# Kernel tuning notes

Measured on AMD Instinct MI355X. Metric: run time of the kernel, lower is better.

Reference implementation:

```python
import jax, jax.numpy as jnp
from jax import lax
import numpy as np

NB_CODE = 16384
DIM = 128
SCALES = [(1, 1), (2, 2), (4, 4), (8, 8), (16, 16)]
PHI_IDX = [0, 1, 1, 2, 3]  # PhiPartiallyShared: argmin(|ticks - si/(SN-1)|), K=4, SN=5
RESI = 0.5  # abs(quant_resi)
BETA = 0.25


def _cubic(x, a=-0.75):
    # PyTorch bicubic kernel (cubic convolution, a=-0.75)
    ax = np.abs(x)
    return np.where(ax <= 1.0, (a + 2.0) * ax ** 3 - (a + 3.0) * ax ** 2 + 1.0,
                    np.where(ax < 2.0, a * ax ** 3 - 5.0 * a * ax ** 2 + 8.0 * a * ax - 4.0 * a, 0.0))


def bicubic_mat(n_in, n_out):
    # 1D interpolation matrix matching torch F.interpolate(mode='bicubic', align_corners=False)
    W = np.zeros((n_out, n_in), dtype=np.float32)
    scale = n_in / n_out
    for i in range(n_out):
        x = (i + 0.5) * scale - 0.5
        x0 = int(np.floor(x))
        t = x - x0
        for k in range(4):
            idx = min(max(x0 - 1 + k, 0), n_in - 1)  # border clamp
            W[i, idx] += _cubic(t + 1.0 - k)
    return jnp.asarray(W)


def phi_apply(h, w, b):
    y = lax.conv_general_dilated(h, w, (1, 1), 'SAME',
                                 dimension_numbers=('NCHW', 'OIHW', 'NCHW'))
    y = y + b[None, :, None, None]
    return h * (1.0 - RESI) + y * RESI


def setup_inputs() -> dict:
    key = jax.random.key(0)
    k1, k2, k3, k4 = jax.random.split(key, 4)
    B, C, J, L = 16, DIM, 16, 16
    f_bcjl = jax.random.normal(k1, (B, C, J, L), dtype=jnp.float32)
    emb = jax.random.normal(k2, (NB_CODE, C), dtype=jnp.float32) * 0.02
    # 4 partially-shared Phi convs (3x3, C->C)
    phi_w = jax.random.normal(k3, (4, C, C, 3, 3), dtype=jnp.float32) * (1.0 / np.sqrt(C * 9))
    phi_b = jax.random.normal(k4, (4, C), dtype=jnp.float32) * 0.01
    return {'f_bcjl': f_bcjl, 'emb': emb, 'phi_w': phi_w, 'phi_b': phi_b}


def reference(f_bcjl, emb, phi_w, phi_b):
    B, C, J, L = f_bcjl.shape
    SN = len(SCALES)
    f_ng = lax.stop_gradient(f_bcjl)
    f_rest = f_ng
    f_hat = jnp.zeros_like(f_ng)
    loss = jnp.float32(0.0)
    e_sq = jnp.sum(emb * emb, axis=1)  # [K]
    idx_all = []
    for si, (sn, tn) in enumerate(SCALES):
        if si != SN - 1:
            # 'area' downsample == integer-factor average pooling here
            r = f_rest.reshape(B, C, sn, J // sn, tn, L // tn).mean(axis=(3, 5))
        else:
            r = f_rest
        rNC = r.transpose(0, 2, 3, 1).reshape(-1, C)  # [N, C]
        d = jnp.sum(rNC * rNC, axis=1, keepdims=True) + e_sq - 2.0 * (rNC @ emb.T)
        idx = jnp.argmin(d, axis=1)  # [N]
        idx_all.append(idx)
        h = emb[idx].reshape(B, sn, tn, C).transpose(0, 3, 1, 2)  # [B,C,sn,tn]
        if si != SN - 1:
            Wj = bicubic_mat(sn, J)
            Wl = bicubic_mat(tn, L)
            h = jnp.einsum('js,bcst,lt->bcjl', Wj, h, Wl)
        k = PHI_IDX[si]
        h = phi_apply(h, phi_w[k], phi_b[k])
        f_hat = f_hat + h
        f_rest = f_rest - h
        loss = loss + BETA * jnp.mean((lax.stop_gradient(f_hat) - f_bcjl) ** 2) \
                    + jnp.mean((f_hat - f_ng) ** 2)
    loss = loss / SN
    idx_cat = jnp.concatenate(idx_all)
    counts = jnp.zeros((NB_CODE,), jnp.float32).at[idx_cat].add(1.0)
    p = counts / idx_cat.shape[0]
    perplexity = jnp.exp(-jnp.sum(p * jnp.log(p + 1e-10)))
    # straight-through estimator
    f_hat_out = lax.stop_gradient(f_hat) - f_ng + f_bcjl
    return (f_hat_out, loss, perplexity)
```

## Files before the change

kernel.cpp:

```cpp
#include <hip/hip_runtime.h>
#include <hip/hip_bf16.h>
#include <math.h>

#define BATCH 16
#define CDIM  128
#define NCODE 16384
#define ELEMS 524288
#define NTOT  5456
#define WEXT_TOT 589824
#define LOSS_COEF 4.76837158203125e-7f

typedef __attribute__((ext_vector_type(8))) short short8;
typedef __attribute__((ext_vector_type(4))) float float4v;
typedef unsigned short ushortT;
typedef unsigned long long u64;
typedef unsigned int u32;

__device__ __forceinline__ ushortT f2bf(float x) {
    __hip_bfloat16 h = __float2bfloat16(x);
    return *reinterpret_cast<ushortT*>(&h);
}
__device__ __forceinline__ float bf2f(ushortT b) {
    __hip_bfloat16 h = *reinterpret_cast<__hip_bfloat16*>(&b);
    return __bfloat162float(h);
}
__device__ __forceinline__ u32 ford(float v) {
    u32 b = __float_as_uint(v);
    return b ^ ((u32)((int)b >> 31) | 0x80000000u);
}

__device__ double cubic_d(double x) {
    const double a = -0.75;
    double ax = fabs(x);
    if (ax <= 1.0) return (a + 2.0) * ax * ax * ax - (a + 3.0) * ax * ax + 1.0;
    if (ax < 2.0)  return a * ax * ax * ax - 5.0 * a * ax * ax + 8.0 * a * ax - 4.0 * a;
    return 0.0;
}

__global__ __launch_bounds__(256)
void k_prologue(const float* __restrict__ f, const float* __restrict__ emb,
                const float* __restrict__ phi_w,
                float* __restrict__ f_rest, float* __restrict__ f_hat,
                float* __restrict__ esq, ushortT* __restrict__ embext,
                ushortT* __restrict__ wext, float* __restrict__ wmat,
                float* __restrict__ lossA, ushortT* __restrict__ rext,
                u64* __restrict__ packed) {
    __shared__ float red[4];
    const int t = threadIdx.x;
    const int bid = blockIdx.x;
    const int id = bid * 256 + t;

    if (bid < 2048) {
        float fv = f[id];
        f_rest[id] = fv;
        f_hat[id] = 0.f;
        int row = id >> 5, c4 = id & 31;
        float4 v = reinterpret_cast<const float4*>(emb + (size_t)row * CDIM)[c4];
        float xs[4] = {v.x, v.y, v.z, v.w};
        ushortT hi[4], lo[4];
        float ss = 0.f;
        #pragma unroll
        for (int i = 0; i < 4; ++i) {
            hi[i] = f2bf(xs[i]);
            lo[i] = f2bf(xs[i] - bf2f(hi[i]));
            ss += xs[i] * xs[i];
        }
        ushortT* base = embext + (size_t)row * 256;
        *reinterpret_cast<ushort4*>(base + c4 * 4)       = make_ushort4(hi[0], hi[1], hi[2], hi[3]);
        *reinterpret_cast<ushort4*>(base + 128 + c4 * 4) = make_ushort4(lo[0], lo[1], lo[2], lo[3]);
        #pragma unroll
        for (int off = 16; off; off >>= 1) ss += __shfl_down(ss, off);
        if ((t & 31) == 0) esq[row] = ss;

        float s = fv;
        #pragma unroll
        for (int off = 32; off; off >>= 1) s += __shfl_down(s, off);
        if ((t & 63) == 0) red[t >> 6] = s;
        __syncthreads();
        if (t == 0) {
            float m = (red[0] + red[1] + red[2] + red[3]) * (1.f / 256.f);
            int b = bid >> 7, c = bid & 127;
            ushortT h = f2bf(m);
            rext[b * 256 + c] = h;
            rext[b * 256 + 128 + c] = f2bf(m - bf2f(h));
        }
    } else {
        int idz = (bid - 2048) * 256 + t;
        if (idz < 30720)
            reinterpret_cast<u32*>(rext + 16 * 256)[idz] = 0;
    }
    if (id < WEXT_TOT) {
        int k4 = id / 147456, rem = id % 147456;
        int co = rem / 1152, kk = rem % 1152;
        int off = kk >> 7, ci = kk & 127;
        float v = 0.5f * phi_w[(((size_t)(k4 * 128 + co)) * 128 + ci) * 9 + off];
        if (ci == co && off == 4) v += 0.5f;
        wext[id] = f2bf(v);
    }
    if (bid == 0 && t < 64) {
        int sIdx = t >> 4;
        int S = 1 << sIdx;
        int j = t & 15;
        const int offs[4] = {0, 16, 48, 112};
        double row[8];
        for (int s = 0; s < 8; ++s) row[s] = 0.0;
        double scale = (double)S / 16.0;
        double x = (j + 0.5) * scale - 0.5;
        double x0 = floor(x);
        double tt = x - x0;
        for (int k = 0; k < 4; ++k) {
            int idx = (int)x0 - 1 + k;
            idx = idx < 0 ? 0 : (idx > S - 1 ? S - 1 : idx);
            row[idx] += cubic_d(tt + 1.0 - k);
        }
        for (int s = 0; s < S; ++s) wmat[offs[sIdx] + j * S + s] = (float)row[s];
    }
    if (id == 0) lossA[0] = 0.f;
    if (id < 8192) packed[id] = ~0ull;
}

__global__ __launch_bounds__(256)
void k_packext(const float* __restrict__ fr, ushortT* __restrict__ re,
               int N, int padN, int S, int lgS) {
    int id = blockIdx.x * 256 + threadIdx.x;
    if (id >= padN * 32) return;
    int row = id >> 5, c4 = id & 31;
    ushortT hi[4], lo[4];
    if (row < N) {
        int mask = S - 1;
        int tt = row & mask, ssi = (row >> lgS) & mask, b = row >> (2 * lgS);
        int bs = 16 >> lgS;
        float inv = 1.f / (float)(bs * bs);
        #pragma unroll
        for (int u = 0; u < 4; ++u) {
            int c = c4 * 4 + u;
            const float* base = fr + (size_t)(b * 128 + c) * 256 + (ssi * bs) * 16 + tt * bs;
            float acc = 0.f;
            for (int jj = 0; jj < bs; ++jj)
                for (int ll = 0; ll < bs; ++ll)
                    acc += base[jj * 16 + ll];
            float x = acc * inv;
            hi[u] = f2bf(x);
            lo[u] = f2bf(x - bf2f(hi[u]));
        }
    } else {
        #pragma unroll
        for (int u = 0; u < 4; ++u) { hi[u] = 0; lo[u] = 0; }
    }
    ushortT* base = re + (size_t)row * 256;
    *reinterpret_cast<ushort4*>(base + c4 * 4)       = make_ushort4(hi[0], hi[1], hi[2], hi[3]);
    *reinterpret_cast<ushort4*>(base + 128 + c4 * 4) = make_ushort4(lo[0], lo[1], lo[2], lo[3]);
}

__global__ __launch_bounds__(256)
void k_packext_wave(const float* __restrict__ fr, ushortT* __restrict__ re,
                    int N, int padN, int S, int lgS) {
    int gid = blockIdx.x * 256 + threadIdx.x;
    int wid = gid >> 6, lane = threadIdx.x & 63;
    if (wid >= padN * 128) return;
    int row = wid >> 7, c = wid & 127;
    float x = 0.f;
    if (row < N) {
        int mask = S - 1;
        int tt = row & mask, ssi = (row >> lgS) & mask, b = row >> (2 * lgS);
        int lgbs = 4 - lgS, bs = 1 << lgbs, cnt = bs * bs;
        const float* base = fr + (size_t)(b * 128 + c) * 256 + (ssi * bs) * 16 + tt * bs;
        float acc = 0.f;
        for (int e = lane; e < cnt; e += 64)
            acc += base[(e >> lgbs) * 16 + (e & (bs - 1))];
        #pragma unroll
        for (int off = 32; off; off >>= 1) acc += __shfl_down(acc, off);
        x = acc / (float)cnt;
    }
    if (lane == 0) {
        ushortT h = f2bf(x);
        re[(size_t)row * 256 + c] = h;
        re[(size_t)row * 256 + 128 + c] = f2bf(x - bf2f(h));
    }
}

__global__ __launch_bounds__(256)
void k_argmin_mfma(const ushortT* __restrict__ rext, const ushortT* __restrict__ embext,
                   const float* __restrict__ esq, int N, int kPerSplit, int KS,
                   u64* __restrict__ packed) {
    __shared__ ushortT Btile[2][64 * 32 * 8];
    const int t = threadIdx.x;
    const int w = t >> 6;
    const int lane = t & 63;
    const int ln = lane & 15;
    const int q  = lane >> 4;
    const int bid = blockIdx.x;
    const int ky = bid % KS;
    const int rb = bid / KS;
    const int k0beg = ky * kPerSplit;
    const int rowW = rb * 128 + w * 32;

    short8 a[2][8];
    #pragma unroll
    for (int ti = 0; ti < 2; ++ti) {
        const ushortT* r0 = rext + (size_t)(rowW + ti * 16 + ln) * 256 + q * 8;
        #pragma unroll
        for (int sb = 0; sb < 8; ++sb)
            a[ti][sb] = *reinterpret_cast<const short8*>(r0 + sb * 32);
    }

    float minv[2][4];
    int   mini[2][4];
    #pragma unroll
    for (int ti = 0; ti < 2; ++ti)
        #pragma unroll
        for (int rg = 0; rg < 4; ++rg) { minv[ti][rg] = 3.4e38f; mini[ti][rg] = 0; }

    const int tiles = kPerSplit >> 6;

    #pragma unroll
    for (int i = 0; i < 8; ++i) {
        int F = (i * 4 + w) * 64 + lane;
        int n = F >> 5, cs = F & 31;
        int cp = (cs & ~7) | ((cs & 7) ^ (n & 7));
        const ushortT* src = embext + (size_t)(k0beg + n) * 256 + cp * 8;
        __builtin_amdgcn_global_load_lds(
            (const __attribute__((address_space(1))) unsigned int*)src,
            (__attribute__((address_space(3))) unsigned int*)&Btile[0][(size_t)((i * 4 + w) * 64) * 8],
            16, 0, 0);
    }

    for (int it = 0; it < tiles; ++it) {
        __syncthreads();
        if (it + 1 < tiles) {
            int k1 = k0beg + (it + 1) * 64;
            int bu = (it + 1) & 1;
            #pragma unroll
            for (int i = 0; i < 8; ++i) {
                int F = (i * 4 + w) * 64 + lane;
                int n = F >> 5, cs = F & 31;
                int cp = (cs & ~7) | ((cs & 7) ^ (n & 7));
                const ushortT* src = embext + (size_t)(k1 + n) * 256 + cp * 8;
                __builtin_amdgcn_global_load_lds(
                    (const __attribute__((address_space(1))) unsigned int*)src,
                    (__attribute__((address_space(3))) unsigned int*)&Btile[bu][(size_t)((i * 4 + w) * 64) * 8],
                    16, 0, 0);
            }
        }
        const ushortT* Bt = Btile[it & 1];
        const int k0 = k0beg + it * 64;

        #pragma unroll
        for (int sub = 0; sub < 4; ++sub) {
            int n = sub * 16 + ln;
            short8 bfr[8];
            #pragma unroll
            for (int sb = 0; sb < 8; ++sb) {
                int cp = q + 4 * sb;
                int cs = (cp & ~7) | ((cp & 7) ^ (n & 7));
                bfr[sb] = *reinterpret_cast<const short8*>(&Bt[(size_t)(n * 32 + cs) * 8]);
            }
            float4v acc[2];
            #pragma unroll
            for (int ti = 0; ti < 2; ++ti) acc[ti] = (float4v){0.f, 0.f, 0.f, 0.f};
            #pragma unroll
            for (int s = 0; s < 12; ++s) {
                int as = s < 8 ? s : s - 8;
                int bs = s < 4 ? s : s - 4;
                #pragma unroll
                for (int ti = 0; ti < 2; ++ti)
                    acc[ti] = __builtin_amdgcn_mfma_f32_16x16x32_bf16(a[ti][as], bfr[bs], acc[ti], 0, 0, 0);
            }
            int kc = k0 + sub * 16 + ln;
            float es = esq[kc];
            #pragma unroll
            for (int ti = 0; ti < 2; ++ti)
                #pragma unroll
                for (int rg = 0; rg < 4; ++rg) {
                    float sc = fmaf(-2.f, acc[ti][rg], es);
                    if (sc < minv[ti][rg]) { minv[ti][rg] = sc; mini[ti][rg] = kc; }
                }
        }
    }

    #pragma unroll
    for (int ti = 0; ti < 2; ++ti)
        #pragma unroll
        for (int rg = 0; rg < 4; ++rg) {
            float v = minv[ti][rg]; int ix = mini[ti][rg];
            #pragma unroll
            for (int off = 1; off < 16; off <<= 1) {
                float ov = __shfl_xor(v, off);
                int   oi = __shfl_xor(ix, off);
                if (ov < v || (ov == v && oi < ix)) { v = ov; ix = oi; }
            }
            if (ln == 0) {
                int row = rowW + ti * 16 + q * 4 + rg;
                if (row < N) {
                    u64 p = ((u64)ford(v) << 32) | (u32)ix;
                    atomicMin(&packed[row], p);
                }
            }
        }
}

__global__ __launch_bounds__(256)
void k_upconv(const float* __restrict__ emb, const u64* __restrict__ packed,
              const float* __restrict__ wm, int S, int lastScale,
              const ushortT* __restrict__ wext, const float* __restrict__ bias,
              const float* __restrict__ f_in, float* __restrict__ f_hat,
              float* __restrict__ f_rest, float* __restrict__ loss_acc,
              int storeRest, int packNext, ushortT* __restrict__ rext_out) {
    __shared__ __align__(16) ushortT Htile[3 * 16 * 128];
    __shared__ __align__(16) float tmpS[3 * 8 * 128];
    __shared__ float wsum[4];
    const int t = threadIdx.x;
    const int b = blockIdx.x >> 4;
    const int j = blockIdx.x & 15;
    const int l = t >> 4, c8 = t & 15;
    const int phys = (c8 & 8) | ((c8 & 7) ^ (l & 7));

    if (lastScale) {
        #pragma unroll
        for (int r = 0; r < 3; ++r) {
            int jin = j - 1 + r;
            float acc[8] = {0.f, 0.f, 0.f, 0.f, 0.f, 0.f, 0.f, 0.f};
            if (jin >= 0 && jin < 16) {
                int idx = (int)(u32)(packed[(b * 16 + jin) * 16 + l] & 0xFFFFFFFFull);
                const float* er = emb + (size_t)idx * CDIM + c8 * 8;
                float4 e0 = *reinterpret_cast<const float4*>(er);
                float4 e1 = *reinterpret_cast<const float4*>(er + 4);
                acc[0] = e0.x; acc[1] = e0.y; acc[2] = e0.z; acc[3] = e0.w;
                acc[4] = e1.x; acc[5] = e1.y; acc[6] = e1.z; acc[7] = e1.w;
            }
            short8 o;
            #pragma unroll
            for (int i = 0; i < 8; ++i) o[i] = (short)f2bf(acc[i]);
            *reinterpret_cast<short8*>(&Htile[((size_t)(r * 16 + l) * 16 + phys) * 8]) = o;
        }
    } else {
        int items = 3 * S * 16;
        for (int i = t; i < items; i += 256) {
            int r = i / (S * 16);
            int rem = i - r * (S * 16);
            int t2 = rem >> 4, cc8 = rem & 15;
            int jin = j - 1 + r;
            float a0[8] = {0.f, 0.f, 0.f, 0.f, 0.f, 0.f, 0.f, 0.f};
            if (jin >= 0 && jin < 16) {
                for (int s = 0; s < S; ++s) {
                    float wjv = wm[jin * S + s];
                    int idx = (int)(u32)(packed[b * S * S + s * S + t2] & 0xFFFFFFFFull);
                    const float* er = emb + (size_t)idx * CDIM + cc8 * 8;
                    float4 e0 = *reinterpret_cast<const float4*>(er);
                    float4 e1 = *reinterpret_cast<const float4*>(er + 4);
                    a0[0] += wjv * e0.x; a0[1] += wjv * e0.y;
                    a0[2] += wjv * e0.z; a0[3] += wjv * e0.w;
                    a0[4] += wjv * e1.x; a0[5] += wjv * e1.y;
                    a0[6] += wjv * e1.z; a0[7] += wjv * e1.w;
                }
            }
            float* tp = &tmpS[((size_t)(r * 8 + t2)) * 128 + cc8 * 8];
            *reinterpret_cast<float4*>(tp)     = make_float4(a0[0], a0[1], a0[2], a0[3]);
            *reinterpret_cast<float4*>(tp + 4) = make_float4(a0[4], a0[5], a0[6], a0[7]);
        }
        __syncthreads();
        #pragma unroll
        for (int r = 0; r < 3; ++r) {
            float acc[8] = {0.f, 0.f, 0.f, 0.f, 0.f, 0.f, 0.f, 0.f};
            for (int t2 = 0; t2 < S; ++t2) {
                float wlv = wm[l * S + t2];
                const float* tp = &tmpS[((size_t)(r * 8 + t2)) * 128 + c8 * 8];
                float4 v0 = *reinterpret_cast<const float4*>(tp);
                float4 v1 = *reinterpret_cast<const float4*>(tp + 4);
                acc[0] += wlv * v0.x; acc[1] += wlv * v0.y;
                acc[2] += wlv * v0.z; acc[3] += wlv * v0.w;
                acc[4] += wlv * v1.x; acc[5] += wlv * v1.y;
                acc[6] += wlv * v1.z; acc[7] += wlv * v1.w;
            }
            short8 o;
            #pragma unroll
            for (int i = 0; i < 8; ++i) o[i] = (short)f2bf(acc[i]);
            *reinterpret_cast<short8*>(&Htile[((size_t)(r * 16 + l) * 16 + phys) * 8]) = o;
        }
    }
    __syncthreads();

    const int w = t >> 6, lane = t & 63;
    const int ln = lane & 15, q = lane >> 4;
    const int co0 = w * 32;
    const ushortT* wA = wext + (size_t)(co0 + ln) * 1152;
    float4v acc2[2] = {{0.f, 0.f, 0.f, 0.f}, {0.f, 0.f, 0.f, 0.f}};
    const short8 zz = {0, 0, 0, 0, 0, 0, 0, 0};

    #pragma unroll 3
    for (int off = 0; off < 9; ++off) {
        const int dj = off / 3, dl = off % 3;
        int cIn = ln + dl - 1;
        int cCl = cIn < 0 ? 0 : (cIn > 15 ? 15 : cIn);
        bool oob = (cIn != cCl);
        int rb = (dj * 16 + cCl) * 128;
        #pragma unroll
        for (int g = 0; g < 4; ++g) {
            int csl = g * 4 + q;
            int ph2 = (csl & 8) | ((csl & 7) ^ (cCl & 7));
            short8 av = *reinterpret_cast<const short8*>(&Htile[rb + ph2 * 8]);
            if (oob) av = zz;
            const ushortT* wr = wA + (off * 4 + g) * 32 + q * 8;
            short8 b0 = *reinterpret_cast<const short8*>(wr);
            short8 b1 = *reinterpret_cast<const short8*>(wr + 16 * 1152);
            acc2[0] = __builtin_amdgcn_mfma_f32_16x16x32_bf16(av, b0, acc2[0], 0, 0, 0);
            acc2[1] = __builtin_amdgcn_mfma_f32_16x16x32_bf16(av, b1, acc2[1], 0, 0, 0);
        }
    }

    float s = 0.f;
    #pragma unroll
    for (int sn = 0; sn < 2; ++sn) {
        int co = co0 + sn * 16 + ln;
        float bsv = 0.5f * bias[co];
        size_t gi = ((size_t)(b * 128 + co) * 16 + j) * 16 + q * 4;
        float4 fh = *reinterpret_cast<const float4*>(&f_hat[gi]);
        float4 fv = *reinterpret_cast<const float4*>(&f_in[gi]);
        float oo[4] = {acc2[sn][0] + bsv, acc2[sn][1] + bsv,
                       acc2[sn][2] + bsv, acc2[sn][3] + bsv};
        float fhv[4] = {fh.x + oo[0], fh.y + oo[1], fh.z + oo[2], fh.w + oo[3]};
        *reinterpret_cast<float4*>(&f_hat[gi]) =
            make_float4(fhv[0], fhv[1], fhv[2], fhv[3]);
        float fvv[4] = {fv.x, fv.y, fv.z, fv.w};
        #pragma unroll
        for (int i = 0; i < 4; ++i) {
            float d = fhv[i] - fvv[i];
            s += d * d;
        }
        if (storeRest || packNext) {
            float4 fr = *reinterpret_cast<const float4*>(&f_rest[gi]);
            float frn[4] = {fr.x - oo[0], fr.y - oo[1], fr.z - oo[2], fr.w - oo[3]};
            if (storeRest)
                *reinterpret_cast<float4*>(&f_rest[gi]) =
                    make_float4(frn[0], frn[1], frn[2], frn[3]);
            if (packNext) {
                #pragma unroll
                for (int i = 0; i < 4; ++i) {
                    int row = b * 256 + j * 16 + q * 4 + i;
                    ushortT hv = f2bf(frn[i]);
                    rext_out[(size_t)row * 256 + co] = hv;
                    rext_out[(size_t)row * 256 + 128 + co] = f2bf(frn[i] - bf2f(hv));
                }
            }
        }
    }
    #pragma unroll
    for (int off = 32; off; off >>= 1) s += __shfl_down(s, off);
    if (lane == 0) wsum[w] = s;
    __syncthreads();
    if (t == 0)
        atomicAdd(loss_acc, (wsum[0] + wsum[1] + wsum[2] + wsum[3]) * LOSS_COEF);
}

__global__ __launch_bounds__(256)
void k_final(const u64* __restrict__ packed, const float* __restrict__ loss_acc,
             float* __restrict__ out) {
    __shared__ u32 cnt2[NCODE / 2];
    __shared__ float ws4[4];
    int t = threadIdx.x;
    for (int i = t; i < NCODE / 2; i += 256) cnt2[i] = 0;
    __syncthreads();
    for (int i = t; i < NTOT; i += 256) {
        int idx = (int)(u32)(packed[i] & 0xFFFFFFFFull);
        atomicAdd(&cnt2[idx >> 1], (idx & 1) ? 65536u : 1u);
    }
    __syncthreads();
    float s = 0.f;
    for (int k = t; k < NCODE; k += 256) {
        u32 c = cnt2[k >> 1];
        c = (k & 1) ? (c >> 16) : (c & 0xFFFFu);
        float p = (float)c * (1.0f / (float)NTOT);
        s += p * logf(p + 1e-10f);
    }
    #pragma unroll
    for (int off = 32; off; off >>= 1) s += __shfl_down(s, off);
    if ((t & 63) == 0) ws4[t >> 6] = s;
    __syncthreads();
    if (t == 0) {
        out[ELEMS]     = loss_acc[0];
        out[ELEMS + 1] = expf(-(ws4[0] + ws4[1] + ws4[2] + ws4[3]));
    }
}

extern "C" void kernel_launch(void* const* d_in, const int* in_sizes, int n_in,
                              void* d_out, int out_size, void* d_ws, size_t ws_size,
                              hipStream_t stream) {
    const float* f     = (const float*)d_in[0];
    const float* emb   = (const float*)d_in[1];
    const float* phi_w = (const float*)d_in[2];
    const float* phi_b = (const float*)d_in[3];
    float* out = (float*)d_out;

    float* wsf = (float*)d_ws;
    float*   f_rest = wsf;
    float*   esq    = wsf + 524288;
    float*   wmat   = wsf + 540672;
    float*   lossA  = wsf + 540928;
    u64*     packed = (u64*)(wsf + 540992);
    ushortT* embext = (ushortT*)(wsf + 557376);
    ushortT* rext   = (ushortT*)(wsf + 2654528);
    ushortT* wext   = (ushortT*)(wsf + 3178816);

    k_prologue<<<2304, 256, 0, stream>>>(f, emb, phi_w, f_rest, out, esq,
                                         embext, wext, wmat, lossA, rext, packed);

    const int Ss[5]     = {1, 2, 4, 8, 16};
    const int lgSs[5]   = {0, 1, 2, 3, 4};
    const int phiIdx[5] = {0, 1, 1, 2, 3};
    const int ksplit[5] = {256, 256, 128, 64, 16};
    const int wmOff[5]  = {0, 16, 48, 112, 0};
    const int pOff[5]   = {0, 16, 80, 336, 1360};

    for (int si = 0; si < 5; ++si) {
        int S = Ss[si], lgS = lgSs[si];
        int N = 16 * S * S;
        int padN = (N + 127) & ~127;
        u64* pk = packed + pOff[si];

        if (si == 1)
            k_packext_wave<<<padN * 128 / 4, 256, 0, stream>>>(f_rest, rext, N, padN, S, lgS);
        else if (si == 2 || si == 3)
            k_packext<<<padN * 32 / 256, 256, 0, stream>>>(f_rest, rext, N, padN, S, lgS);

        int KS = ksplit[si];
        k_argmin_mfma<<<(padN / 128) * KS, 256, 0, stream>>>(rext, embext, esq,
                                                             N, NCODE / KS, KS, pk);

        int k = phiIdx[si];
        k_upconv<<<256, 256, 0, stream>>>(emb, pk, wmat + wmOff[si], S, si == 4 ? 1 : 0,
                                          wext + (size_t)k * 147456,
                                          phi_b + (size_t)k * 128, f, out, f_rest, lossA,
                                          si <= 2 ? 1 : 0, si == 3 ? 1 : 0, rext);
    }

    k_final<<<1, 256, 0, stream>>>(packed, lossA, out);
}
```

Measured before the change: 320.2 us.

## Fuse all stages into one persistent cooperative kernel with grid syncs

Replaces the chain of roughly fifteen kernel launches (prologue, pack, argmin, upconv per scale, final) with a single cooperative persistent kernel that loops over jobs and uses grid.sync between stages. The goal is to remove launch overhead and inter-kernel gaps, which are large relative to the small per-scale work. The argmin's double-buffered LDS prefetch is dropped for a single buffer so the shared memory fits two blocks per CU, which gives up overlap between loads and MFMA work. The old multi-kernel path stays as a fallback if the cooperative launch is unavailable or fails.

```diff
diff --git a/kernel.cpp b/kernel.cpp
--- a/kernel.cpp
+++ b/kernel.cpp
@@ -1,8 +1,10 @@
 #include <hip/hip_runtime.h>
+#include <hip/hip_cooperative_groups.h>
 #include <hip/hip_bf16.h>
 #include <math.h>
 
-#define BATCH 16
+namespace cg = cooperative_groups;
+
 #define CDIM  128
 #define NCODE 16384
 #define ELEMS 524288
@@ -28,7 +30,6 @@
     u32 b = __float_as_uint(v);
     return b ^ ((u32)((int)b >> 31) | 0x80000000u);
 }
-
 __device__ double cubic_d(double x) {
     const double a = -0.75;
     double ax = fabs(x);
@@ -37,161 +38,18 @@
     return 0.0;
 }
 
-__global__ __launch_bounds__(256)
-void k_prologue(const float* __restrict__ f, const float* __restrict__ emb,
-                const float* __restrict__ phi_w,
-                float* __restrict__ f_rest, float* __restrict__ f_hat,
-                float* __restrict__ esq, ushortT* __restrict__ embext,
-                ushortT* __restrict__ wext, float* __restrict__ wmat,
-                float* __restrict__ lossA, ushortT* __restrict__ rext,
-                u64* __restrict__ packed) {
-    __shared__ float red[4];
-    const int t = threadIdx.x;
-    const int bid = blockIdx.x;
-    const int id = bid * 256 + t;
-
-    if (bid < 2048) {
-        float fv = f[id];
-        f_rest[id] = fv;
-        f_hat[id] = 0.f;
-        int row = id >> 5, c4 = id & 31;
-        float4 v = reinterpret_cast<const float4*>(emb + (size_t)row * CDIM)[c4];
-        float xs[4] = {v.x, v.y, v.z, v.w};
-        ushortT hi[4], lo[4];
-        float ss = 0.f;
-        #pragma unroll
-        for (int i = 0; i < 4; ++i) {
-            hi[i] = f2bf(xs[i]);
-            lo[i] = f2bf(xs[i] - bf2f(hi[i]));
-            ss += xs[i] * xs[i];
-        }
-        ushortT* base = embext + (size_t)row * 256;
-        *reinterpret_cast<ushort4*>(base + c4 * 4)       = make_ushort4(hi[0], hi[1], hi[2], hi[3]);
-        *reinterpret_cast<ushort4*>(base + 128 + c4 * 4) = make_ushort4(lo[0], lo[1], lo[2], lo[3]);
-        #pragma unroll
-        for (int off = 16; off; off >>= 1) ss += __shfl_down(ss, off);
-        if ((t & 31) == 0) esq[row] = ss;
-
-        float s = fv;
-        #pragma unroll
-        for (int off = 32; off; off >>= 1) s += __shfl_down(s, off);
-        if ((t & 63) == 0) red[t >> 6] = s;
-        __syncthreads();
-        if (t == 0) {
-            float m = (red[0] + red[1] + red[2] + red[3]) * (1.f / 256.f);
-            int b = bid >> 7, c = bid & 127;
-            ushortT h = f2bf(m);
-            rext[b * 256 + c] = h;
-            rext[b * 256 + 128 + c] = f2bf(m - bf2f(h));
-        }
-    } else {
-        int idz = (bid - 2048) * 256 + t;
-        if (idz < 30720)
-            reinterpret_cast<u32*>(rext + 16 * 256)[idz] = 0;
-    }
-    if (id < WEXT_TOT) {
-        int k4 = id / 147456, rem = id % 147456;
-        int co = rem / 1152, kk = rem % 1152;
-        int off = kk >> 7, ci = kk & 127;
-        float v = 0.5f * phi_w[(((size_t)(k4 * 128 + co)) * 128 + ci) * 9 + off];
-        if (ci == co && off == 4) v += 0.5f;
-        wext[id] = f2bf(v);
-    }
-    if (bid == 0 && t < 64) {
-        int sIdx = t >> 4;
-        int S = 1 << sIdx;
-        int j = t & 15;
-        const int offs[4] = {0, 16, 48, 112};
-        double row[8];
-        for (int s = 0; s < 8; ++s) row[s] = 0.0;
-        double scale = (double)S / 16.0;
-        double x = (j + 0.5) * scale - 0.5;
-        double x0 = floor(x);
-        double tt = x - x0;
-        for (int k = 0; k < 4; ++k) {
-            int idx = (int)x0 - 1 + k;
-            idx = idx < 0 ? 0 : (idx > S - 1 ? S - 1 : idx);
-            row[idx] += cubic_d(tt + 1.0 - k);
-        }
-        for (int s = 0; s < S; ++s) wmat[offs[sIdx] + j * S + s] = (float)row[s];
-    }
-    if (id == 0) lossA[0] = 0.f;
-    if (id < 8192) packed[id] = ~0ull;
-}
-
-__global__ __launch_bounds__(256)
-void k_packext(const float* __restrict__ fr, ushortT* __restrict__ re,
-               int N, int padN, int S, int lgS) {
-    int id = blockIdx.x * 256 + threadIdx.x;
-    if (id >= padN * 32) return;
-    int row = id >> 5, c4 = id & 31;
-    ushortT hi[4], lo[4];
-    if (row < N) {
-        int mask = S - 1;
-        int tt = row & mask, ssi = (row >> lgS) & mask, b = row >> (2 * lgS);
-        int bs = 16 >> lgS;
-        float inv = 1.f / (float)(bs * bs);
-        #pragma unroll
-        for (int u = 0; u < 4; ++u) {
-            int c = c4 * 4 + u;
-            const float* base = fr + (size_t)(b * 128 + c) * 256 + (ssi * bs) * 16 + tt * bs;
-            float acc = 0.f;
-            for (int jj = 0; jj < bs; ++jj)
-                for (int ll = 0; ll < bs; ++ll)
-                    acc += base[jj * 16 + ll];
-            float x = acc * inv;
-            hi[u] = f2bf(x);
-            lo[u] = f2bf(x - bf2f(hi[u]));
-        }
-    } else {
-        #pragma unroll
-        for (int u = 0; u < 4; ++u) { hi[u] = 0; lo[u] = 0; }
-    }
-    ushortT* base = re + (size_t)row * 256;
-    *reinterpret_cast<ushort4*>(base + c4 * 4)       = make_ushort4(hi[0], hi[1], hi[2], hi[3]);
-    *reinterpret_cast<ushort4*>(base + 128 + c4 * 4) = make_ushort4(lo[0], lo[1], lo[2], lo[3]);
-}
-
-__global__ __launch_bounds__(256)
-void k_packext_wave(const float* __restrict__ fr, ushortT* __restrict__ re,
-                    int N, int padN, int S, int lgS) {
-    int gid = blockIdx.x * 256 + threadIdx.x;
-    int wid = gid >> 6, lane = threadIdx.x & 63;
-    if (wid >= padN * 128) return;
-    int row = wid >> 7, c = wid & 127;
-    float x = 0.f;
-    if (row < N) {
-        int mask = S - 1;
-        int tt = row & mask, ssi = (row >> lgS) & mask, b = row >> (2 * lgS);
-        int lgbs = 4 - lgS, bs = 1 << lgbs, cnt = bs * bs;
-        const float* base = fr + (size_t)(b * 128 + c) * 256 + (ssi * bs) * 16 + tt * bs;
-        float acc = 0.f;
-        for (int e = lane; e < cnt; e += 64)
-            acc += base[(e >> lgbs) * 16 + (e & (bs - 1))];
-        #pragma unroll
-        for (int off = 32; off; off >>= 1) acc += __shfl_down(acc, off);
-        x = acc / (float)cnt;
-    }
-    if (lane == 0) {
-        ushortT h = f2bf(x);
-        re[(size_t)row * 256 + c] = h;
-        re[(size_t)row * 256 + 128 + c] = f2bf(x - bf2f(h));
-    }
-}
-
-__global__ __launch_bounds__(256)
-void k_argmin_mfma(const ushortT* __restrict__ rext, const ushortT* __restrict__ embext,
-                   const float* __restrict__ esq, int N, int kPerSplit, int KS,
-                   u64* __restrict__ packed) {
-    __shared__ ushortT Btile[2][64 * 32 * 8];
-    const int t = threadIdx.x;
+
+__device__ __forceinline__
+void dev_argmin_sb(char* smem, int jid, const ushortT* __restrict__ rext,
+                   const ushortT* __restrict__ embext, const float* __restrict__ esq,
+                   int N, int kPerSplit, int KS, u64* __restrict__ packed, int t) {
+    ushortT* B0 = reinterpret_cast<ushortT*>(smem);
     const int w = t >> 6;
     const int lane = t & 63;
     const int ln = lane & 15;
     const int q  = lane >> 4;
-    const int bid = blockIdx.x;
-    const int ky = bid % KS;
-    const int rb = bid / KS;
+    const int ky = jid % KS;
+    const int rb = jid / KS;
     const int k0beg = ky * kPerSplit;
     const int rowW = rb * 128 + w * 32;
 
@@ -212,38 +70,21 @@
         for (int rg = 0; rg < 4; ++rg) { minv[ti][rg] = 3.4e38f; mini[ti][rg] = 0; }
 
     const int tiles = kPerSplit >> 6;
-
-    #pragma unroll
-    for (int i = 0; i < 8; ++i) {
-        int F = (i * 4 + w) * 64 + lane;
-        int n = F >> 5, cs = F & 31;
-        int cp = (cs & ~7) | ((cs & 7) ^ (n & 7));
-        const ushortT* src = embext + (size_t)(k0beg + n) * 256 + cp * 8;
-        __builtin_amdgcn_global_load_lds(
-            (const __attribute__((address_space(1))) unsigned int*)src,
-            (__attribute__((address_space(3))) unsigned int*)&Btile[0][(size_t)((i * 4 + w) * 64) * 8],
-            16, 0, 0);
-    }
-
     for (int it = 0; it < tiles; ++it) {
         __syncthreads();
-        if (it + 1 < tiles) {
-            int k1 = k0beg + (it + 1) * 64;
-            int bu = (it + 1) & 1;
-            #pragma unroll
-            for (int i = 0; i < 8; ++i) {
-                int F = (i * 4 + w) * 64 + lane;
-                int n = F >> 5, cs = F & 31;
-                int cp = (cs & ~7) | ((cs & 7) ^ (n & 7));
-                const ushortT* src = embext + (size_t)(k1 + n) * 256 + cp * 8;
-                __builtin_amdgcn_global_load_lds(
-                    (const __attribute__((address_space(1))) unsigned int*)src,
-                    (__attribute__((address_space(3))) unsigned int*)&Btile[bu][(size_t)((i * 4 + w) * 64) * 8],
-                    16, 0, 0);
-            }
-        }
-        const ushortT* Bt = Btile[it & 1];
-        const int k0 = k0beg + it * 64;
+        int k0 = k0beg + it * 64;
+        #pragma unroll
+        for (int i = 0; i < 8; ++i) {
+            int F = (i * 4 + w) * 64 + lane;
+            int n = F >> 5, cs = F & 31;
+            int cp = (cs & ~7) | ((cs & 7) ^ (n & 7));
+            const ushortT* src = embext + (size_t)(k0 + n) * 256 + cp * 8;
+            __builtin_amdgcn_global_load_lds(
+                (const __attribute__((address_space(1))) unsigned int*)src,
+                (__attribute__((address_space(3))) unsigned int*)&B0[(size_t)((i * 4 + w) * 64) * 8],
+                16, 0, 0);
+        }
+        __syncthreads();
 
         #pragma unroll
         for (int sub = 0; sub < 4; ++sub) {
@@ -253,7 +94,7 @@
             for (int sb = 0; sb < 8; ++sb) {
                 int cp = q + 4 * sb;
                 int cs = (cp & ~7) | ((cp & 7) ^ (n & 7));
-                bfr[sb] = *reinterpret_cast<const short8*>(&Bt[(size_t)(n * 32 + cs) * 8]);
+                bfr[sb] = *reinterpret_cast<const short8*>(&B0[(size_t)(n * 32 + cs) * 8]);
             }
             float4v acc[2];
             #pragma unroll
@@ -299,19 +140,19 @@
         }
 }
 
-__global__ __launch_bounds__(256)
-void k_upconv(const float* __restrict__ emb, const u64* __restrict__ packed,
-              const float* __restrict__ wm, int S, int lastScale,
-              const ushortT* __restrict__ wext, const float* __restrict__ bias,
-              const float* __restrict__ f_in, float* __restrict__ f_hat,
-              float* __restrict__ f_rest, float* __restrict__ loss_acc,
-              int storeRest, int packNext, ushortT* __restrict__ rext_out) {
-    __shared__ __align__(16) ushortT Htile[3 * 16 * 128];
-    __shared__ __align__(16) float tmpS[3 * 8 * 128];
-    __shared__ float wsum[4];
-    const int t = threadIdx.x;
-    const int b = blockIdx.x >> 4;
-    const int j = blockIdx.x & 15;
+__device__ __forceinline__
+void dev_upconv(char* smem, int job, const float* __restrict__ emb,
+                const u64* __restrict__ packed, const float* __restrict__ wm,
+                int S, int lastScale, const ushortT* __restrict__ wext,
+                const float* __restrict__ bias, const float* __restrict__ f_in,
+                float* __restrict__ f_hat, float* __restrict__ f_rest,
+                float* __restrict__ loss_acc, int storeRest, int packNext,
+                ushortT* __restrict__ rext_out, int t) {
+    ushortT* Htile = reinterpret_cast<ushortT*>(smem);
+    float*   tmpS  = reinterpret_cast<float*>(smem + 12288);
+    float*   wsum  = reinterpret_cast<float*>(smem + 24576);
+    const int b = job >> 4;
+    const int j = job & 15;
     const int l = t >> 4, c8 = t & 15;
     const int phys = (c8 & 8) | ((c8 & 7) ^ (l & 7));
 
@@ -452,6 +293,375 @@
         atomicAdd(loss_acc, (wsum[0] + wsum[1] + wsum[2] + wsum[3]) * LOSS_COEF);
 }
 
+__global__ __launch_bounds__(256, 2)
+void k_mega(const float* __restrict__ f, const float* __restrict__ emb,
+            const float* __restrict__ phi_w, const float* __restrict__ phi_b,
+            float* __restrict__ out, float* __restrict__ f_rest,
+            float* __restrict__ esq, float* __restrict__ wmat,
+            float* __restrict__ lossA, u64* __restrict__ packed,
+            ushortT* __restrict__ embext, ushortT* __restrict__ rext,
+            ushortT* __restrict__ wext) {
+    cg::grid_group grid = cg::this_grid();
+    __shared__ __align__(16) char smem[32768];
+    const int t = threadIdx.x;
+    const int bid = blockIdx.x;
+    const int NB = gridDim.x;
+
+    {
+        float* red = reinterpret_cast<float*>(smem);
+        for (int base = bid * 256; base < WEXT_TOT; base += NB * 256) {
+            int id = base + t;
+            if (base < ELEMS) {
+                float fv = f[id];
+                f_rest[id] = fv;
+                out[id] = 0.f;
+                int row = id >> 5, c4 = id & 31;
+                float4 v = reinterpret_cast<const float4*>(emb + (size_t)row * CDIM)[c4];
+                float xs[4] = {v.x, v.y, v.z, v.w};
+                ushortT hi[4], lo[4];
+                float ss = 0.f;
+                #pragma unroll
+                for (int i = 0; i < 4; ++i) {
+                    hi[i] = f2bf(xs[i]);
+                    lo[i] = f2bf(xs[i] - bf2f(hi[i]));
+                    ss += xs[i] * xs[i];
+                }
+                ushortT* basep = embext + (size_t)row * 256;
+                *reinterpret_cast<ushort4*>(basep + c4 * 4)       = make_ushort4(hi[0], hi[1], hi[2], hi[3]);
+                *reinterpret_cast<ushort4*>(basep + 128 + c4 * 4) = make_ushort4(lo[0], lo[1], lo[2], lo[3]);
+                #pragma unroll
+                for (int off = 16; off; off >>= 1) ss += __shfl_down(ss, off);
+                if ((t & 31) == 0) esq[row] = ss;
+
+                float s = fv;
+                #pragma unroll
+                for (int off = 32; off; off >>= 1) s += __shfl_down(s, off);
+                if ((t & 63) == 0) red[t >> 6] = s;
+                __syncthreads();
+                if (t == 0) {
+                    float m = (red[0] + red[1] + red[2] + red[3]) * (1.f / 256.f);
+                    int plane = base >> 8;
+                    int b = plane >> 7, c = plane & 127;
+                    ushortT h = f2bf(m);
+                    rext[b * 256 + c] = h;
+                    rext[b * 256 + 128 + c] = f2bf(m - bf2f(h));
+                }
+                __syncthreads();
+            }
+            if (id < WEXT_TOT) {
+                int k4 = id / 147456, rem = id % 147456;
+                int co = rem / 1152, kk = rem % 1152;
+                int off = kk >> 7, ci = kk & 127;
+                float v = 0.5f * phi_w[(((size_t)(k4 * 128 + co)) * 128 + ci) * 9 + off];
+                if (ci == co && off == 4) v += 0.5f;
+                wext[id] = f2bf(v);
+            }
+        }
+        for (int idz = bid * 256 + t; idz < 30720; idz += NB * 256)
+            reinterpret_cast<u32*>(rext + 16 * 256)[idz] = 0;
+        if (bid == 0 && t < 64) {
+            int sIdx = t >> 4;
+            int S = 1 << sIdx;
+            int j = t & 15;
+            const int offs[4] = {0, 16, 48, 112};
+            double row[8];
+            for (int s = 0; s < 8; ++s) row[s] = 0.0;
+            double scale = (double)S / 16.0;
+            double x = (j + 0.5) * scale - 0.5;
+            double x0 = floor(x);
+            double tt = x - x0;
+            for (int k = 0; k < 4; ++k) {
+                int idx = (int)x0 - 1 + k;
+                idx = idx < 0 ? 0 : (idx > S - 1 ? S - 1 : idx);
+                row[idx] += cubic_d(tt + 1.0 - k);
+            }
+            for (int s = 0; s < S; ++s) wmat[offs[sIdx] + j * S + s] = (float)row[s];
+        }
+        if (bid == 0 && t == 0) lossA[0] = 0.f;
+        for (int i = bid * 256 + t; i < 8192; i += NB * 256) packed[i] = ~0ull;
+    }
+    grid.sync();
+
+    const int Ss[5]     = {1, 2, 4, 8, 16};
+    const int phiIdx[5] = {0, 1, 1, 2, 3};
+    const int ksplit[5] = {256, 256, 128, 64, 16};
+    const int wmOff[5]  = {0, 16, 48, 112, 0};
+    const int pOff[5]   = {0, 16, 80, 336, 1360};
+    const int padNs[5]  = {128, 128, 256, 1024, 4096};
+
+    for (int si = 0; si < 5; ++si) {
+        const int S = Ss[si];
+        const int N = 16 * S * S;
+        const int padN = padNs[si];
+        const int KS = ksplit[si];
+        u64* pk = packed + pOff[si];
+
+        if (si == 1) {
+            const int w = t >> 6, lane = t & 63;
+            for (int wj = bid * 4 + w; wj < padN * 128; wj += NB * 4) {
+                int row = wj >> 7, c = wj & 127;
+                float x = 0.f;
+                if (row < N) {
+                    int tt = row & 1, ssi = (row >> 1) & 1, b = row >> 2;
+                    const float* basep = f_rest + (size_t)(b * 128 + c) * 256 + (ssi * 8) * 16 + tt * 8;
+                    float acc = 0.f;
+                    for (int e = lane; e < 64; e += 64)
+                        acc += basep[(e >> 3) * 16 + (e & 7)];
+                    #pragma unroll
+                    for (int off = 32; off; off >>= 1) acc += __shfl_down(acc, off);
+                    x = acc * (1.f / 64.f);
+                }
+                if (lane == 0) {
+                    ushortT h = f2bf(x);
+                    rext[(size_t)row * 256 + c] = h;
+                    rext[(size_t)row * 256 + 128 + c] = f2bf(x - bf2f(h));
+                }
+            }
+            grid.sync();
+        } else if (si == 2 || si == 3) {
+            const int lgS = si;
+            for (int id2 = bid * 256 + t; id2 < padN * 32; id2 += NB * 256) {
+                int row = id2 >> 5, c4 = id2 & 31;
+                ushortT hi[4], lo[4];
+                if (row < N) {
+                    int mask = S - 1;
+                    int tt = row & mask, ssi = (row >> lgS) & mask, b = row >> (2 * lgS);
+                    int bs = 16 >> lgS;
+                    float inv = 1.f / (float)(bs * bs);
+                    #pragma unroll
+                    for (int u = 0; u < 4; ++u) {
+                        int c = c4 * 4 + u;
+                        const float* basep = f_rest + (size_t)(b * 128 + c) * 256 + (ssi * bs) * 16 + tt * bs;
+                        float acc = 0.f;
+                        for (int jj = 0; jj < bs; ++jj)
+                            for (int ll = 0; ll < bs; ++ll)
+                                acc += basep[jj * 16 + ll];
+                        float x = acc * inv;
+                        hi[u] = f2bf(x);
+                        lo[u] = f2bf(x - bf2f(hi[u]));
+                    }
+                } else {
+                    #pragma unroll
+                    for (int u = 0; u < 4; ++u) { hi[u] = 0; lo[u] = 0; }
+                }
+                ushortT* basep = rext + (size_t)row * 256;
+                *reinterpret_cast<ushort4*>(basep + c4 * 4)       = make_ushort4(hi[0], hi[1], hi[2], hi[3]);
+                *reinterpret_cast<ushort4*>(basep + 128 + c4 * 4) = make_ushort4(lo[0], lo[1], lo[2], lo[3]);
+            }
+            grid.sync();
+        }
+
+        {
+            int njobs = (padN / 128) * KS;
+            for (int jid = bid; jid < njobs; jid += NB)
+                dev_argmin_sb(smem, jid, rext, embext, esq, N, NCODE / KS, KS, pk, t);
+            grid.sync();
+        }
+
+        {
+            int k = phiIdx[si];
+            for (int job = bid; job < 256; job += NB)
+                dev_upconv(smem, job, emb, pk, wmat + wmOff[si], S, si == 4 ? 1 : 0,
+                           wext + (size_t)k * 147456, phi_b + (size_t)k * 128,
+                           f, out, f_rest, lossA,
+                           si <= 2 ? 1 : 0, si == 3 ? 1 : 0, rext, t);
+            grid.sync();
+        }
+    }
+
+    if (bid == 0) {
+        u32* cnt2 = reinterpret_cast<u32*>(smem);
+        for (int i = t; i < NCODE / 2; i += 256) cnt2[i] = 0;
+        __syncthreads();
+        for (int i = t; i < NTOT; i += 256) {
+            int idx = (int)(u32)(packed[i] & 0xFFFFFFFFull);
+            atomicAdd(&cnt2[idx >> 1], (idx & 1) ? 65536u : 1u);
+        }
+        __syncthreads();
+        float s = 0.f;
+        for (int k = t; k < NCODE; k += 256) {
+            u32 c = cnt2[k >> 1];
+            c = (k & 1) ? (c >> 16) : (c & 0xFFFFu);
+            float p = (float)c * (1.0f / (float)NTOT);
+            s += p * logf(p + 1e-10f);
+        }
+        __syncthreads();
+        float* ws4 = reinterpret_cast<float*>(smem);
+        #pragma unroll
+        for (int off = 32; off; off >>= 1) s += __shfl_down(s, off);
+        if ((t & 63) == 0) ws4[t >> 6] = s;
+        __syncthreads();
+        if (t == 0) {
+            out[ELEMS]     = lossA[0];
+            out[ELEMS + 1] = expf(-(ws4[0] + ws4[1] + ws4[2] + ws4[3]));
+        }
+    }
+}
+
+__global__ __launch_bounds__(256)
+void k_prologue(const float* __restrict__ f, const float* __restrict__ emb,
+                const float* __restrict__ phi_w,
+                float* __restrict__ f_rest, float* __restrict__ f_hat,
+                float* __restrict__ esq, ushortT* __restrict__ embext,
+                ushortT* __restrict__ wext, float* __restrict__ wmat,
+                float* __restrict__ lossA, ushortT* __restrict__ rext,
+                u64* __restrict__ packed) {
+    __shared__ float red[4];
+    const int t = threadIdx.x;
+    const int bid = blockIdx.x;
+    const int id = bid * 256 + t;
+
+    if (bid < 2048) {
+        float fv = f[id];
+        f_rest[id] = fv;
+        f_hat[id] = 0.f;
+        int row = id >> 5, c4 = id & 31;
+        float4 v = reinterpret_cast<const float4*>(emb + (size_t)row * CDIM)[c4];
+        float xs[4] = {v.x, v.y, v.z, v.w};
+        ushortT hi[4], lo[4];
+        float ss = 0.f;
+        #pragma unroll
+        for (int i = 0; i < 4; ++i) {
+            hi[i] = f2bf(xs[i]);
+            lo[i] = f2bf(xs[i] - bf2f(hi[i]));
+            ss += xs[i] * xs[i];
+        }
+        ushortT* base = embext + (size_t)row * 256;
+        *reinterpret_cast<ushort4*>(base + c4 * 4)       = make_ushort4(hi[0], hi[1], hi[2], hi[3]);
+        *reinterpret_cast<ushort4*>(base + 128 + c4 * 4) = make_ushort4(lo[0], lo[1], lo[2], lo[3]);
+        #pragma unroll
+        for (int off = 16; off; off >>= 1) ss += __shfl_down(ss, off);
+        if ((t & 31) == 0) esq[row] = ss;
+
+        float s = fv;
+        #pragma unroll
+        for (int off = 32; off; off >>= 1) s += __shfl_down(s, off);
+        if ((t & 63) == 0) red[t >> 6] = s;
+        __syncthreads();
+        if (t == 0) {
+            float m = (red[0] + red[1] + red[2] + red[3]) * (1.f / 256.f);
+            int b = bid >> 7, c = bid & 127;
+            ushortT h = f2bf(m);
+            rext[b * 256 + c] = h;
+            rext[b * 256 + 128 + c] = f2bf(m - bf2f(h));
+        }
+    } else {
+        int idz = (bid - 2048) * 256 + t;
+        if (idz < 30720)
+            reinterpret_cast<u32*>(rext + 16 * 256)[idz] = 0;
+    }
+    if (id < WEXT_TOT) {
+        int k4 = id / 147456, rem = id % 147456;
+        int co = rem / 1152, kk = rem % 1152;
+        int off = kk >> 7, ci = kk & 127;
+        float v = 0.5f * phi_w[(((size_t)(k4 * 128 + co)) * 128 + ci) * 9 + off];
+        if (ci == co && off == 4) v += 0.5f;
+        wext[id] = f2bf(v);
+    }
+    if (bid == 0 && t < 64) {
+        int sIdx = t >> 4;
+        int S = 1 << sIdx;
+        int j = t & 15;
+        const int offs[4] = {0, 16, 48, 112};
+        double row[8];
+        for (int s = 0; s < 8; ++s) row[s] = 0.0;
+        double scale = (double)S / 16.0;
+        double x = (j + 0.5) * scale - 0.5;
+        double x0 = floor(x);
+        double tt = x - x0;
+        for (int k = 0; k < 4; ++k) {
+            int idx = (int)x0 - 1 + k;
+            idx = idx < 0 ? 0 : (idx > S - 1 ? S - 1 : idx);
+            row[idx] += cubic_d(tt + 1.0 - k);
+        }
+        for (int s = 0; s < S; ++s) wmat[offs[sIdx] + j * S + s] = (float)row[s];
+    }
+    if (id == 0) lossA[0] = 0.f;
+    if (id < 8192) packed[id] = ~0ull;
+}
+
+__global__ __launch_bounds__(256)
+void k_packext(const float* __restrict__ fr, ushortT* __restrict__ re,
+               int N, int padN, int S, int lgS) {
+    int id = blockIdx.x * 256 + threadIdx.x;
+    if (id >= padN * 32) return;
+    int row = id >> 5, c4 = id & 31;
+    ushortT hi[4], lo[4];
+    if (row < N) {
+        int mask = S - 1;
+        int tt = row & mask, ssi = (row >> lgS) & mask, b = row >> (2 * lgS);
+        int bs = 16 >> lgS;
+        float inv = 1.f / (float)(bs * bs);
+        #pragma unroll
+        for (int u = 0; u < 4; ++u) {
+            int c = c4 * 4 + u;
+            const float* base = fr + (size_t)(b * 128 + c) * 256 + (ssi * bs) * 16 + tt * bs;
+            float acc = 0.f;
+            for (int jj = 0; jj < bs; ++jj)
+                for (int ll = 0; ll < bs; ++ll)
+                    acc += base[jj * 16 + ll];
+            float x = acc * inv;
+            hi[u] = f2bf(x);
+            lo[u] = f2bf(x - bf2f(hi[u]));
+        }
+    } else {
+        #pragma unroll
+        for (int u = 0; u < 4; ++u) { hi[u] = 0; lo[u] = 0; }
+    }
+    ushortT* base = re + (size_t)row * 256;
+    *reinterpret_cast<ushort4*>(base + c4 * 4)       = make_ushort4(hi[0], hi[1], hi[2], hi[3]);
+    *reinterpret_cast<ushort4*>(base + 128 + c4 * 4) = make_ushort4(lo[0], lo[1], lo[2], lo[3]);
+}
+
+__global__ __launch_bounds__(256)
+void k_packext_wave(const float* __restrict__ fr, ushortT* __restrict__ re,
+                    int N, int padN, int S, int lgS) {
+    int gid = blockIdx.x * 256 + threadIdx.x;
+    int wid = gid >> 6, lane = threadIdx.x & 63;
+    if (wid >= padN * 128) return;
+    int row = wid >> 7, c = wid & 127;
+    float x = 0.f;
+    if (row < N) {
+        int mask = S - 1;
+        int tt = row & mask, ssi = (row >> lgS) & mask, b = row >> (2 * lgS);
+        int lgbs = 4 - lgS, bs = 1 << lgbs, cnt = bs * bs;
+        const float* base = fr + (size_t)(b * 128 + c) * 256 + (ssi * bs) * 16 + tt * bs;
+        float acc = 0.f;
+        for (int e = lane; e < cnt; e += 64)
+            acc += base[(e >> lgbs) * 16 + (e & (bs - 1))];
+        #pragma unroll
+        for (int off = 32; off; off >>= 1) acc += __shfl_down(acc, off);
+        x = acc / (float)cnt;
+    }
+    if (lane == 0) {
+        ushortT h = f2bf(x);
+        re[(size_t)row * 256 + c] = h;
+        re[(size_t)row * 256 + 128 + c] = f2bf(x - bf2f(h));
+    }
+}
+
+__global__ __launch_bounds__(256)
+void k_argmin_fb(const ushortT* __restrict__ rext, const ushortT* __restrict__ embext,
+                 const float* __restrict__ esq, int N, int kPerSplit, int KS,
+                 u64* __restrict__ packed) {
+    __shared__ __align__(16) char smem[32768];
+    dev_argmin_sb(smem, blockIdx.x, rext, embext, esq, N, kPerSplit, KS, packed,
+                  threadIdx.x);
+}
+
+__global__ __launch_bounds__(256)
+void k_upconv_fb(const float* __restrict__ emb, const u64* __restrict__ packed,
+                 const float* __restrict__ wm, int S, int lastScale,
+                 const ushortT* __restrict__ wext, const float* __restrict__ bias,
+                 const float* __restrict__ f_in, float* __restrict__ f_hat,
+                 float* __restrict__ f_rest, float* __restrict__ loss_acc,
+                 int storeRest, int packNext, ushortT* __restrict__ rext_out) {
+    __shared__ __align__(16) char smem[24592];
+    dev_upconv(smem, blockIdx.x, emb, packed, wm, S, lastScale, wext, bias,
+               f_in, f_hat, f_rest, loss_acc, storeRest, packNext, rext_out,
+               threadIdx.x);
+}
+
 __global__ __launch_bounds__(256)
 void k_final(const u64* __restrict__ packed, const float* __restrict__ loss_acc,
              float* __restrict__ out) {
@@ -501,37 +711,54 @@
     ushortT* rext   = (ushortT*)(wsf + 2654528);
     ushortT* wext   = (ushortT*)(wsf + 3178816);
 
-    k_prologue<<<2304, 256, 0, stream>>>(f, emb, phi_w, f_rest, out, esq,
-                                         embext, wext, wmat, lossA, rext, packed);
-
-    const int Ss[5]     = {1, 2, 4, 8, 16};
-    const int lgSs[5]   = {0, 1, 2, 3, 4};
-    const int phiIdx[5] = {0, 1, 1, 2, 3};
-    const int ksplit[5] = {256, 256, 128, 64, 16};
-    const int wmOff[5]  = {0, 16, 48, 112, 0};
-    const int pOff[5]   = {0, 16, 80, 336, 1360};
-
-    for (int si = 0; si < 5; ++si) {
-        int S = Ss[si], lgS = lgSs[si];
-        int N = 16 * S * S;
-        int padN = (N + 127) & ~127;
-        u64* pk = packed + pOff[si];
-
-        if (si == 1)
-            k_packext_wave<<<padN * 128 / 4, 256, 0, stream>>>(f_rest, rext, N, padN, S, lgS);
-        else if (si == 2 || si == 3)
-            k_packext<<<padN * 32 / 256, 256, 0, stream>>>(f_rest, rext, N, padN, S, lgS);
-
-        int KS = ksplit[si];
-        k_argmin_mfma<<<(padN / 128) * KS, 256, 0, stream>>>(rext, embext, esq,
-                                                             N, NCODE / KS, KS, pk);
-
-        int k = phiIdx[si];
-        k_upconv<<<256, 256, 0, stream>>>(emb, pk, wmat + wmOff[si], S, si == 4 ? 1 : 0,
-                                          wext + (size_t)k * 147456,
-                                          phi_b + (size_t)k * 128, f, out, f_rest, lossA,
-                                          si <= 2 ? 1 : 0, si == 3 ? 1 : 0, rext);
-    }
-
-    k_final<<<1, 256, 0, stream>>>(packed, lossA, out);
-}
+    int coop = 0, dev = 0, nbPerCU = 0;
+    hipError_t e0 = hipGetDevice(&dev);
+    hipError_t e1 = hipDeviceGetAttribute(&coop, hipDeviceAttributeCooperativeLaunch, dev);
+    hipError_t qerr = hipOccupancyMaxActiveBlocksPerMultiprocessor(
+        &nbPerCU, k_mega, 256, 0);
+    int gridN = nbPerCU * 256;
+    if (gridN > 512) gridN = 512;
+
+    hipError_t lerr = hipErrorUnknown;
+    if (e0 == hipSuccess && e1 == hipSuccess && coop &&
+        qerr == hipSuccess && gridN >= 128) {
+        void* args[] = {
+            (void*)&f, (void*)&emb, (void*)&phi_w, (void*)&phi_b, (void*)&out,
+            (void*)&f_rest, (void*)&esq, (void*)&wmat, (void*)&lossA,
+            (void*)&packed, (void*)&embext, (void*)&rext, (void*)&wext
+        };
+        lerr = hipLaunchCooperativeKernel((const void*)k_mega, dim3(gridN),
+                                          dim3(256), args, 0, stream);
+    }
+    if (lerr != hipSuccess) {
+        k_prologue<<<2304, 256, 0, stream>>>(f, emb, phi_w, f_rest, out, esq,
+                                             embext, wext, wmat, lossA, rext, packed);
+        const int Ss[5]     = {1, 2, 4, 8, 16};
+        const int lgSs[5]   = {0, 1, 2, 3, 4};
+        const int phiIdx[5] = {0, 1, 1, 2, 3};
+        const int ksplit[5] = {256, 256, 128, 64, 16};
+        const int wmOff[5]  = {0, 16, 48, 112, 0};
+        const int pOff[5]   = {0, 16, 80, 336, 1360};
+        for (int si = 0; si < 5; ++si) {
+            int S = Ss[si], lgS = lgSs[si];
+            int N = 16 * S * S;
+            int padN = (N + 127) & ~127;
+            u64* pk = packed + pOff[si];
+            if (si == 1)
+                k_packext_wave<<<padN * 128 / 4, 256, 0, stream>>>(f_rest, rext, N, padN, S, lgS);
+            else if (si == 2 || si == 3)
+                k_packext<<<padN * 32 / 256, 256, 0, stream>>>(f_rest, rext, N, padN, S, lgS);
+            int KS = ksplit[si];
+            k_argmin_fb<<<(padN / 128) * KS, 256, 0, stream>>>(rext, embext, esq,
+                                                               N, NCODE / KS, KS, pk);
+            int k = phiIdx[si];
+            k_upconv_fb<<<256, 256, 0, stream>>>(emb, pk, wmat + wmOff[si], S,
+                                                 si == 4 ? 1 : 0,
+                                                 wext + (size_t)k * 147456,
+                                                 phi_b + (size_t)k * 128, f, out,
+                                                 f_rest, lossA,
+                                                 si <= 2 ? 1 : 0, si == 3 ? 1 : 0, rext);
+        }
+        k_final<<<1, 256, 0, stream>>>(packed, lossA, out);
+    }
+}
```

Result: slower. 676.7 us (+111.3%).
